# Optimization experiments

Measured on AMD Instinct MI355X. Metric: run time of the kernel, lower is better.

## Reference

```python
import jax, jax.numpy as jnp
import numpy as np

N = 100000   # graph nodes
E = 600000   # edges
D = 128      # feature_dim
K = 3        # candidate ops per MixedOp
EPS = 1e-5   # BatchNorm eps


def _param_stack(key, n_ops):
    kW, kb = jax.random.split(key)
    W = jax.random.normal(kW, (n_ops, K, D, D), jnp.float32) * (1.0 / np.sqrt(D))
    b = jax.random.normal(kb, (n_ops, K, D), jnp.float32) * 0.01
    g = jnp.ones((n_ops, K, D), jnp.float32)
    be = jnp.zeros((n_ops, K, D), jnp.float32)
    return W, b, g, be


def setup_inputs() -> dict:
    key = jax.random.key(0)
    ks = jax.random.split(key, 16)
    inp = {
        'src_emb': jax.random.normal(ks[0], (N, D), jnp.float32),
        'hr': jax.random.normal(ks[1], (N, D), jnp.float32),
        'edge_src': jax.random.randint(ks[2], (E,), 0, N),
        'edge_dst': jax.random.randint(ks[3], (E,), 0, N),
        'weights_zero': jax.random.uniform(ks[4], (1, K), jnp.float32),
        'weights_first': jax.random.uniform(ks[5], (3, K), jnp.float32),
        'weights_middle': jax.random.uniform(ks[6], (2, K), jnp.float32),
        'weights_last': jax.random.uniform(ks[7], (2, K), jnp.float32),
    }
    for name, k, n_ops in [('zero', ks[8], 1), ('first', ks[9], 3), ('mid', ks[10], 2), ('last', ks[11], 2)]:
        W, b, g, be = _param_stack(k, n_ops)
        inp[f'W_{name}'] = W; inp[f'b_{name}'] = b
        inp[f'g_{name}'] = g; inp[f'be_{name}'] = be
    inp['W_cat'] = jax.random.normal(ks[12], (3 * D, D), jnp.float32) * (1.0 / np.sqrt(3 * D))
    inp['b_cat'] = jax.random.normal(ks[13], (D,), jnp.float32) * 0.01
    inp['g_cat'] = jnp.ones((D,), jnp.float32)
    inp['be_cat'] = jnp.zeros((D,), jnp.float32)
    return inp


def _mean_agg(h, src, dst):
    s = jax.ops.segment_sum(h[src], dst, num_segments=N)            # [N,D]
    deg = jax.ops.segment_sum(jnp.ones((src.shape[0],), h.dtype), dst, num_segments=N)
    return s / jnp.maximum(deg, 1.0)[:, None]


def _max_agg(h, src, dst):
    m = jax.ops.segment_max(h[src], dst, num_segments=N)            # -inf for empty segs
    return jnp.where(jnp.isfinite(m), m, 0.0)


def _mixed(cands, w, W, b, g, be):
    # cands: list of K [N,D]; w:[K]; W:[K,D,D]; b/g/be:[K,D]
    x = jnp.stack(cands)                                            # [K,N,D]
    y = jnp.einsum('knd,kdf->knf', x, W) + b[:, None, :]            # Linear per candidate
    mu = jnp.mean(y, axis=1, keepdims=True)                         # BatchNorm1d (batch stats)
    var = jnp.var(y, axis=1, keepdims=True)
    y = (y - mu) * jax.lax.rsqrt(var + EPS) * g[:, None, :] + be[:, None, :]
    y = jax.nn.relu(y)
    return jnp.einsum('k,knd->nd', w, y)                            # alpha-weighted sum


def _graph_cands(h, src, dst):
    return [h, _mean_agg(h, src, dst), _max_agg(h, src, dst)]


def _cell_forward(src_emb, hr, edge_src, edge_dst,
                  weights_zero, weights_first, weights_middle, weights_last,
                  W_zero, b_zero, g_zero, be_zero,
                  W_first, b_first, g_first, be_first,
                  W_mid, b_mid, g_mid, be_mid,
                  W_last, b_last, g_last, be_last,
                  W_cat, b_cat, g_cat, be_cat):
    src, dst = edge_src, edge_dst
    # Cell_Zero: relation-composition candidates on (src_emb, hr)
    pre = [src_emb, src_emb - hr, src_emb * hr]
    h_in = _mixed(pre, weights_zero[0], W_zero[0], b_zero[0], g_zero[0], be_zero[0])
    # Cell_First (nodes=2): ops layout [(i=0,j=0),(i=1,j=0),(i=1,j=1)]
    states = [h_in]
    s0 = _mixed(_graph_cands(states[0], src, dst), weights_first[0], W_first[0], b_first[0], g_first[0], be_first[0])
    states.append(s0)
    s1 = (_mixed(_graph_cands(states[0], src, dst), weights_first[1], W_first[1], b_first[1], g_first[1], be_first[1])
          + _mixed(_graph_cands(states[1], src, dst), weights_first[2], W_first[2], b_first[2], g_first[2], be_first[2]))
    states.append(s1)
    states = states[1:]                                             # drop h_in -> len 2
    # Cell_Middle (nodes=2): one MixedOp per state
    states = [_mixed(_graph_cands(states[i], src, dst), weights_middle[i], W_mid[i], b_mid[i], g_mid[i], be_mid[i])
              for i in range(2)]
    # Cell_Last (in_nodes=2, nodes=1): one new state from both inputs; returns all 3
    s_last = (_mixed(_graph_cands(states[0], src, dst), weights_last[0], W_last[0], b_last[0], g_last[0], be_last[0])
              + _mixed(_graph_cands(states[1], src, dst), weights_last[1], W_last[1], b_last[1], g_last[1], be_last[1]))
    states = states + [s_last]                                      # len 3
    # concat -> Linear -> BN -> ReLU (dropout p=0)
    h = jnp.concatenate(states, axis=1) @ W_cat + b_cat             # [N,D]
    mu = jnp.mean(h, axis=0, keepdims=True)
    var = jnp.var(h, axis=0, keepdims=True)
    h = (h - mu) * jax.lax.rsqrt(var + EPS) * g_cat + be_cat
    return jax.nn.relu(h)


def reference(src_emb, hr, edge_src, edge_dst,
              weights_zero, weights_first, weights_middle, weights_last,
              W_zero, b_zero, g_zero, be_zero,
              W_first, b_first, g_first, be_first,
              W_mid, b_mid, g_mid, be_mid,
              W_last, b_last, g_last, be_last,
              W_cat, b_cat, g_cat, be_cat):
    return _cell_forward(src_emb, hr, edge_src, edge_dst,
                         weights_zero, weights_first, weights_middle, weights_last,
                         W_zero, b_zero, g_zero, be_zero,
                         W_first, b_first, g_first, be_first,
                         W_mid, b_mid, g_mid, be_mid,
                         W_last, b_last, g_last, be_last,
                         W_cat, b_cat, g_cat, be_cat)
```

## Files before the change

kernel.cpp:

```cpp
#include <hip/hip_runtime.h>

#define N_NODES 100000
#define N_EDGES 600000
#define NPAD    100096
#define NTILES  782
#define SCAN_B  98
#define EPS_F   1e-5f
#define GRIDG   256

typedef __bf16 bf16_t;
typedef __bf16 bf16x8 __attribute__((ext_vector_type(8)));
typedef __bf16 bf16x4 __attribute__((ext_vector_type(4)));
typedef float  f32x4  __attribute__((ext_vector_type(4)));

__global__ __launch_bounds__(256)
void init_zero_kernel(int* __restrict__ deg, int* __restrict__ cnt)
{
    int i = blockIdx.x * 256 + threadIdx.x;
    if (i < N_NODES) deg[i] = 0;
    if (i < 32) cnt[i] = 0;
}

__global__ __launch_bounds__(256)
void transpose_w_kernel(const float* __restrict__ Wz, const float* __restrict__ Wf,
                        const float* __restrict__ Wm, const float* __restrict__ Wl,
                        const float* __restrict__ Wc, bf16_t* __restrict__ wt)
{
    int idx = blockIdx.x * 256 + threadIdx.x;
    int mat = idx >> 14;
    int off = idx & 16383;
    int n = off >> 7, kk = off & 127;
    const float* src;
    if      (mat < 3)  src = Wz + mat * 16384;
    else if (mat < 12) src = Wf + (mat - 3) * 16384;
    else if (mat < 18) src = Wm + (mat - 12) * 16384;
    else if (mat < 24) src = Wl + (mat - 18) * 16384;
    else               src = Wc + (mat - 24) * 16384;
    wt[idx] = (bf16_t)src[kk * 128 + n];
}

__global__ __launch_bounds__(256)
void pre_kernel(const float* __restrict__ se, const float* __restrict__ hr,
                bf16_t* __restrict__ p0, bf16_t* __restrict__ p1, bf16_t* __restrict__ p2)
{
    long i = ((long)blockIdx.x * 256 + threadIdx.x) * 8;
    float4 a0 = *(const float4*)&se[i], a1 = *(const float4*)&se[i + 4];
    float4 b0 = *(const float4*)&hr[i], b1 = *(const float4*)&hr[i + 4];
    float av[8] = {a0.x, a0.y, a0.z, a0.w, a1.x, a1.y, a1.z, a1.w};
    float bv[8] = {b0.x, b0.y, b0.z, b0.w, b1.x, b1.y, b1.z, b1.w};
    bf16x8 o0, o1, o2;
#pragma unroll
    for (int j = 0; j < 8; ++j) {
        o0[j] = (bf16_t)av[j];
        o1[j] = (bf16_t)(av[j] - bv[j]);
        o2[j] = (bf16_t)(av[j] * bv[j]);
    }
    *(bf16x8*)&p0[i] = o0;
    *(bf16x8*)&p1[i] = o1;
    *(bf16x8*)&p2[i] = o2;
}

__global__ __launch_bounds__(256)
void deg_count_kernel(const int* __restrict__ dst, int* __restrict__ deg)
{
    int i = blockIdx.x * 256 + threadIdx.x;
    if (i < N_EDGES) atomicAdd(&deg[dst[i]], 1);
}

__global__ __launch_bounds__(256)
void scan_a_kernel(const int* __restrict__ deg, int* __restrict__ partials)
{
    __shared__ int ls[256];
    int b = blockIdx.x, t = threadIdx.x;
    int s = 0;
    for (int j = 0; j < 4; ++j) {
        int i = b * 1024 + t * 4 + j;
        if (i < N_NODES) s += deg[i];
    }
    ls[t] = s; __syncthreads();
    for (int o = 128; o > 0; o >>= 1) {
        if (t < o) ls[t] += ls[t + o];
        __syncthreads();
    }
    if (t == 0) partials[b] = ls[0];
}

__global__ void scan_b_kernel(const int* __restrict__ partials, int* __restrict__ pofs)
{
    if (threadIdx.x == 0) {
        int a = 0;
        for (int i = 0; i < SCAN_B; ++i) { pofs[i] = a; a += partials[i]; }
    }
}

__global__ __launch_bounds__(256)
void scan_c_kernel(const int* __restrict__ deg, const int* __restrict__ pofs,
                   int* __restrict__ row_ptr, int* __restrict__ cursor)
{
    __shared__ int ls[256];
    int b = blockIdx.x, t = threadIdx.x;
    int v[4], s = 0;
    for (int j = 0; j < 4; ++j) {
        int i = b * 1024 + t * 4 + j;
        v[j] = (i < N_NODES) ? deg[i] : 0;
        s += v[j];
    }
    ls[t] = s; __syncthreads();
    for (int o = 1; o < 256; o <<= 1) {
        int tv = (t >= o) ? ls[t - o] : 0;
        __syncthreads();
        ls[t] += tv;
        __syncthreads();
    }
    int excl = ls[t] - s + pofs[b];
    for (int j = 0; j < 4; ++j) {
        int i = b * 1024 + t * 4 + j;
        if (i < N_NODES) { row_ptr[i] = excl; cursor[i] = excl; excl += v[j]; }
    }
    if (b == 0 && t == 0) row_ptr[N_NODES] = N_EDGES;
}

__global__ __launch_bounds__(256)
void scatter_kernel(const int* __restrict__ src, const int* __restrict__ dst,
                    int* __restrict__ cursor, int* __restrict__ csr_src)
{
    int i = blockIdx.x * 256 + threadIdx.x;
    if (i < N_EDGES) {
        int p = atomicAdd(&cursor[dst[i]], 1);
        csr_src[p] = src[i];
    }
}

__global__ __launch_bounds__(256)
void agg_kernel(const bf16_t* __restrict__ h, const int* __restrict__ row_ptr,
                const int* __restrict__ csr_src,
                bf16_t* __restrict__ mean_o, bf16_t* __restrict__ max_o)
{
    int node = blockIdx.x * 16 + (threadIdx.x >> 4);
    int dd = (threadIdx.x & 15) * 8;
    int e0 = row_ptr[node], e1 = row_ptr[node + 1];
    float s[8], mx[8];
#pragma unroll
    for (int j = 0; j < 8; ++j) { s[j] = 0.f; mx[j] = 0.f; }
    for (int e = e0; e < e1; ++e) {
        int sc = csr_src[e];
        bf16x8 v = *(const bf16x8*)&h[(long)sc * 128 + dd];
#pragma unroll
        for (int j = 0; j < 8; ++j) {
            float f = (float)v[j];
            s[j] += f;
            mx[j] = fmaxf(mx[j], f);
        }
    }
    float inv = 1.f / fmaxf((float)(e1 - e0), 1.f);
    bf16x8 om, ox;
#pragma unroll
    for (int j = 0; j < 8; ++j) { om[j] = (bf16_t)(s[j] * inv); ox[j] = (bf16_t)mx[j]; }
    *(bf16x8*)&mean_o[(long)node * 128 + dd] = om;
    *(bf16x8*)&max_o [(long)node * 128 + dd] = ox;
}

__device__ __forceinline__ void gload_lds16(const bf16_t* g, bf16_t* l)
{
    __builtin_amdgcn_global_load_lds(
        (const __attribute__((address_space(1))) void*)g,
        (__attribute__((address_space(3))) void*)l, 16, 0, 0);
}

__device__ __forceinline__ void barrier_lgkm()
{
    asm volatile("s_waitcnt lgkmcnt(0)" ::: "memory");
    __builtin_amdgcn_s_barrier();
    asm volatile("" ::: "memory");
}

__device__ __forceinline__ void grid_bar(int* c, int do_rel, int do_acq)
{
    __syncthreads();
    if (threadIdx.x == 0) {
        if (do_rel) __builtin_amdgcn_fence(__ATOMIC_RELEASE, "agent");
        __hip_atomic_fetch_add(c, 1, __ATOMIC_RELAXED, __HIP_MEMORY_SCOPE_AGENT);
        while (__hip_atomic_load(c, __ATOMIC_RELAXED, __HIP_MEMORY_SCOPE_AGENT) < GRIDG)
            __builtin_amdgcn_s_sleep(16);
        if (do_acq) __builtin_amdgcn_fence(__ATOMIC_ACQUIRE, "agent");
    }
    __syncthreads();
}

__global__ __launch_bounds__(512, 1)
void mixed_kernel(const bf16_t* __restrict__ x0, const bf16_t* __restrict__ x1,
                  const bf16_t* __restrict__ x2, const bf16_t* __restrict__ wt,
                  const float* __restrict__ bias, const float* __restrict__ gg,
                  const float* __restrict__ be, const float* __restrict__ wmix,
                  bf16_t* __restrict__ outb, float* __restrict__ outf,
                  float* __restrict__ partial, float* __restrict__ tmp,
                  int* __restrict__ cnt, int mode, int accflag)
{
    __shared__ __align__(16) bf16_t lds_w[2][16384];
    __shared__ __align__(16) bf16_t lds_x[2][16384];
    __shared__ float lsc[768];

    const int tid  = threadIdx.x;
    const int lane = tid & 63;
    const int w8   = tid >> 6;
    const int quad = lane >> 4;
    const int t16  = lane & 15;
    const int wr = w8 >> 2, wc = w8 & 3;
    const int bid = blockIdx.x;
    const float invN = 1.0f / (float)N_NODES;

    int srcoff[4], dsto[4];
#pragma unroll
    for (int i = 0; i < 4; ++i) {
        int ci = i * 512 + tid;
        int row = ci >> 4, c = ci & 15;
        srcoff[i] = row * 128 + ((c ^ (row & 15)) * 8);
        dsto[i]   = ci * 8;
    }
    auto stage = [&](const bf16_t* src, bf16_t* dst) {
#pragma unroll
        for (int i = 0; i < 4; ++i)
            gload_lds16(src + srcoff[i], dst + dsto[i]);
    };
    auto xp = [&](int c) { return (c == 0) ? x0 : (c == 1) ? x1 : x2; };

    const int ts = (int)(((long)bid * NTILES) / GRIDG);
    const int te = (int)(((long)(bid + 1) * NTILES) / GRIDG);
    const int nk = (mode == 0) ? 3 : 1;

    f32x4 acc[2][4];

    {
        int s, e;
        if (mode == 0) {
            s = (int)(((long)bid * (NTILES * 3)) / GRIDG);
            e = (int)(((long)(bid + 1) * (NTILES * 3)) / GRIDG);
        } else {
            s = ts * 3; e = te * 3;
        }
        auto kofA = [&](int w) { return (mode == 0) ? (w / NTILES) : (w % 3); };
        auto tofA = [&](int w) { return (mode == 0) ? (w % NTILES) : (w / 3); };
        auto wslA = [&](int w, int k) { return (mode == 0) ? (k & 1) : (w & 1); };

        {
            int k0 = kofA(s);
            stage(wt + (long)k0 * 16384, lds_w[wslA(s, k0)]);
            stage(xp(k0) + (long)tofA(s) * 16384, lds_x[s & 1]);
        }
        for (int w = s; w < e; ++w) {
            const int ksel = kofA(w), tile = tofA(w);
            const bf16_t* wb = lds_w[wslA(w, ksel)];
            const bf16_t* xb = lds_x[w & 1];

            __syncthreads();
            if (w + 1 < e) {
                int kn = kofA(w + 1), tn = tofA(w + 1);
                if (mode == 1 || kn != ksel)
                    stage(wt + (long)kn * 16384, lds_w[wslA(w + 1, kn)]);
                stage(xp(kn) + (long)tn * 16384, lds_x[(w + 1) & 1]);
            }
            if (mode == 0 || ksel == 0) {
#pragma unroll
                for (int a = 0; a < 2; ++a)
#pragma unroll
                    for (int b = 0; b < 4; ++b) acc[a][b] = (f32x4){0.f, 0.f, 0.f, 0.f};
            }
#pragma unroll
            for (int ks = 0; ks < 4; ++ks) {
                bf16x8 xf[4], wf[2];
#pragma unroll
                for (int ms = 0; ms < 4; ++ms) {
                    int row = wr * 64 + ms * 16 + t16;
                    int sw = (ks * 4 + quad) ^ t16;
                    xf[ms] = *(const bf16x8*)&xb[row * 128 + sw * 8];
                }
#pragma unroll
                for (int ns = 0; ns < 2; ++ns) {
                    int row = wc * 32 + ns * 16 + t16;
                    int sw = (ks * 4 + quad) ^ t16;
                    wf[ns] = *(const bf16x8*)&wb[row * 128 + sw * 8];
                }
#pragma unroll
                for (int ns = 0; ns < 2; ++ns)
#pragma unroll
                    for (int ms = 0; ms < 4; ++ms)
                        acc[ns][ms] = __builtin_amdgcn_mfma_f32_16x16x32_bf16(
                            wf[ns], xf[ms], acc[ns][ms], 0, 0, 0);
            }
            if (mode == 0 || ksel == 2) {
                const float* bp = bias + ((mode == 0) ? ksel * 128 : 0);
                float ss[8], sq[8];
#pragma unroll
                for (int i = 0; i < 8; ++i) { ss[i] = 0.f; sq[i] = 0.f; }
#pragma unroll
                for (int ms = 0; ms < 4; ++ms) {
                    long m = (long)tile * 128 + wr * 64 + ms * 16 + t16;
                    if (m < N_NODES) {
#pragma unroll
                        for (int ns = 0; ns < 2; ++ns) {
                            int n0 = wc * 32 + ns * 16 + quad * 4;
                            float4 b4 = *(const float4*)&bp[n0];
                            float v0 = acc[ns][ms][0] + b4.x;
                            float v1 = acc[ns][ms][1] + b4.y;
                            float v2 = acc[ns][ms][2] + b4.z;
                            float v3 = acc[ns][ms][3] + b4.w;
                            ss[ns * 4 + 0] += v0; sq[ns * 4 + 0] += v0 * v0;
                            ss[ns * 4 + 1] += v1; sq[ns * 4 + 1] += v1 * v1;
                            ss[ns * 4 + 2] += v2; sq[ns * 4 + 2] += v2 * v2;
                            ss[ns * 4 + 3] += v3; sq[ns * 4 + 3] += v3 * v3;
                        }
                    }
                }
#pragma unroll
                for (int o = 1; o < 16; o <<= 1) {
#pragma unroll
                    for (int i = 0; i < 8; ++i) {
                        ss[i] += __shfl_xor(ss[i], o);
                        sq[i] += __shfl_xor(sq[i], o);
                    }
                }
                if (t16 == 0) {
#pragma unroll
                    for (int ns = 0; ns < 2; ++ns)
#pragma unroll
                        for (int i = 0; i < 4; ++i) {
                            lsc[w8 * 64 +      ns * 16 + quad * 4 + i] = ss[ns * 4 + i];
                            lsc[w8 * 64 + 32 + ns * 16 + quad * 4 + i] = sq[ns * 4 + i];
                        }
                }
                barrier_lgkm();
                if (tid < 256) {
                    int selo = (tid >> 7) * 32;
                    int d = tid & 127;
                    int wcq = d >> 5, f = d & 31;
                    float v = lsc[wcq * 64 + selo + f] + lsc[(wcq + 4) * 64 + selo + f];
                    int slice = (mode == 0) ? ksel : 0;
                    partial[((long)slice * NTILES + tile) * 256 + tid] = v;
                }
            }
        }
    }

    const int foldblk = (bid < nk * 16);
    grid_bar(cnt + 0, 1, foldblk);
    if (foldblk && tid < 256) {
        int k = bid >> 4, j = bid & 15;
        int b0 = j * 49, b1 = (b0 + 49 < NTILES) ? b0 + 49 : NTILES;
        float s = 0.f;
        const float* pp = partial + (long)k * NTILES * 256 + tid;
        for (int b = b0; b < b1; ++b) s += pp[(long)b * 256];
        tmp[(k * 16 + j) * 256 + tid] = s;
    }
    grid_bar(cnt + 1, foldblk, 1);
    if (tid < 128) {
        for (int k = 0; k < nk; ++k) {
            float S = 0.f, Q = 0.f;
#pragma unroll
            for (int j = 0; j < 16; ++j) {
                S += tmp[(k * 16 + j) * 256 + tid];
                Q += tmp[(k * 16 + j) * 256 + 128 + tid];
            }
            float mu = S * invN;
            float var = Q * invN - mu * mu;
            float rs = rsqrtf(var + EPS_F);
            float gk = gg[k * 128 + tid], bek = be[k * 128 + tid];
            float bk = bias[k * 128 + tid];
            float wk = (mode == 0) ? wmix[k] : 1.f;
            lsc[k * 256 + tid]       = wk * rs * gk;
            lsc[k * 256 + 128 + tid] = wk * ((bk - mu) * rs * gk + bek);
        }
    }
    __syncthreads();

    {
        int tile = ts, c = 0, p = 0;
        const int w0 = ts * 3, w1 = te * 3;
        f32x4 res[2][4];
        stage(wt, lds_w[0]);
        stage(x0 + (long)ts * 16384, lds_x[0]);
        for (int w = w0; w < w1; ++w) {
            __syncthreads();
            int cn = c + 1, tn = tile;
            if (cn == 3) { cn = 0; tn = tile + 1; }
            if (w + 1 < w1) {
                stage(wt + (long)cn * 16384, lds_w[p ^ 1]);
                stage(xp(cn) + (long)tn * 16384, lds_x[p ^ 1]);
            }
            if (mode == 0 || c == 0) {
#pragma unroll
                for (int a = 0; a < 2; ++a)
#pragma unroll
                    for (int b = 0; b < 4; ++b) acc[a][b] = (f32x4){0.f, 0.f, 0.f, 0.f};
            }
            if (mode == 0 && c == 0) {
                if (accflag) {
#pragma unroll
                    for (int ns = 0; ns < 2; ++ns)
#pragma unroll
                        for (int ms = 0; ms < 4; ++ms) {
                            long m = (long)tile * 128 + wr * 64 + ms * 16 + t16;
                            int n0 = wc * 32 + ns * 16 + quad * 4;
                            bf16x4 pv = *(const bf16x4*)&outb[m * 128 + n0];
                            res[ns][ms] = (f32x4){(float)pv[0], (float)pv[1],
                                                  (float)pv[2], (float)pv[3]};
                        }
                } else {
#pragma unroll
                    for (int a = 0; a < 2; ++a)
#pragma unroll
                        for (int b = 0; b < 4; ++b) res[a][b] = (f32x4){0.f, 0.f, 0.f, 0.f};
                }
            }
#pragma unroll
            for (int ks = 0; ks < 4; ++ks) {
                bf16x8 xf[4], wf[2];
#pragma unroll
                for (int ms = 0; ms < 4; ++ms) {
                    int row = wr * 64 + ms * 16 + t16;
                    int sw = (ks * 4 + quad) ^ t16;
                    xf[ms] = *(const bf16x8*)&lds_x[p][row * 128 + sw * 8];
                }
#pragma unroll
                for (int ns = 0; ns < 2; ++ns) {
                    int row = wc * 32 + ns * 16 + t16;
                    int sw = (ks * 4 + quad) ^ t16;
                    wf[ns] = *(const bf16x8*)&lds_w[p][row * 128 + sw * 8];
                }
#pragma unroll
                for (int ns = 0; ns < 2; ++ns)
#pragma unroll
                    for (int ms = 0; ms < 4; ++ms)
                        acc[ns][ms] = __builtin_amdgcn_mfma_f32_16x16x32_bf16(
                            wf[ns], xf[ms], acc[ns][ms], 0, 0, 0);
            }
            if (mode == 0) {
#pragma unroll
                for (int ns = 0; ns < 2; ++ns) {
                    int n0 = wc * 32 + ns * 16 + quad * 4;
                    float4 A4 = *(const float4*)&lsc[c * 256 + n0];
                    float4 B4 = *(const float4*)&lsc[c * 256 + 128 + n0];
#pragma unroll
                    for (int ms = 0; ms < 4; ++ms) {
                        res[ns][ms][0] += fmaxf(acc[ns][ms][0] * A4.x + B4.x, 0.f);
                        res[ns][ms][1] += fmaxf(acc[ns][ms][1] * A4.y + B4.y, 0.f);
                        res[ns][ms][2] += fmaxf(acc[ns][ms][2] * A4.z + B4.z, 0.f);
                        res[ns][ms][3] += fmaxf(acc[ns][ms][3] * A4.w + B4.w, 0.f);
                    }
                }
                if (c == 2) {
#pragma unroll
                    for (int ms = 0; ms < 4; ++ms) {
                        long m = (long)tile * 128 + wr * 64 + ms * 16 + t16;
                        if (m < N_NODES) {
#pragma unroll
                            for (int ns = 0; ns < 2; ++ns) {
                                int n0 = wc * 32 + ns * 16 + quad * 4;
                                bf16x4 ov;
                                ov[0] = (bf16_t)res[ns][ms][0];
                                ov[1] = (bf16_t)res[ns][ms][1];
                                ov[2] = (bf16_t)res[ns][ms][2];
                                ov[3] = (bf16_t)res[ns][ms][3];
                                *(bf16x4*)&outb[m * 128 + n0] = ov;
                            }
                        }
                    }
                }
            } else if (c == 2) {
#pragma unroll
                for (int ms = 0; ms < 4; ++ms) {
                    long m = (long)tile * 128 + wr * 64 + ms * 16 + t16;
                    if (m < N_NODES) {
#pragma unroll
                        for (int ns = 0; ns < 2; ++ns) {
                            int n0 = wc * 32 + ns * 16 + quad * 4;
                            float4 A4 = *(const float4*)&lsc[n0];
                            float4 B4 = *(const float4*)&lsc[128 + n0];
                            float4 o;
                            o.x = fmaxf(acc[ns][ms][0] * A4.x + B4.x, 0.f);
                            o.y = fmaxf(acc[ns][ms][1] * A4.y + B4.y, 0.f);
                            o.z = fmaxf(acc[ns][ms][2] * A4.z + B4.z, 0.f);
                            o.w = fmaxf(acc[ns][ms][3] * A4.w + B4.w, 0.f);
                            *(float4*)&outf[m * 128 + n0] = o;
                        }
                    }
                }
            }
            p ^= 1; c = cn; tile = tn;
        }
    }
}

extern "C" void kernel_launch(void* const* d_in, const int* in_sizes, int n_in,
                              void* d_out, int out_size, void* d_ws, size_t ws_size,
                              hipStream_t stream)
{
    const float* src_emb = (const float*)d_in[0];
    const float* hr      = (const float*)d_in[1];
    const int*   e_src   = (const int*)d_in[2];
    const int*   e_dst   = (const int*)d_in[3];
    const float* w_zero  = (const float*)d_in[4];
    const float* w_first = (const float*)d_in[5];
    const float* w_mid   = (const float*)d_in[6];
    const float* w_last  = (const float*)d_in[7];
    const float* W_zero  = (const float*)d_in[8];
    const float* b_zero  = (const float*)d_in[9];
    const float* g_zero  = (const float*)d_in[10];
    const float* be_zero = (const float*)d_in[11];
    const float* W_first = (const float*)d_in[12];
    const float* b_first = (const float*)d_in[13];
    const float* g_first = (const float*)d_in[14];
    const float* be_first= (const float*)d_in[15];
    const float* W_mid   = (const float*)d_in[16];
    const float* b_mid   = (const float*)d_in[17];
    const float* g_mid   = (const float*)d_in[18];
    const float* be_mid  = (const float*)d_in[19];
    const float* W_last  = (const float*)d_in[20];
    const float* b_last  = (const float*)d_in[21];
    const float* g_last  = (const float*)d_in[22];
    const float* be_last = (const float*)d_in[23];
    const float* W_cat   = (const float*)d_in[24];
    const float* b_cat   = (const float*)d_in[25];
    const float* g_cat   = (const float*)d_in[26];
    const float* be_cat  = (const float*)d_in[27];
    float* out = (float*)d_out;

    char* ws = (char*)d_ws;
    size_t off = 0;
    auto carve = [&](size_t bytes) -> char* {
        off = (off + 255) & ~(size_t)255;
        char* p = ws + off;
        off += bytes;
        return p;
    };

    const size_t SB = (size_t)NPAD * 128 * sizeof(bf16_t);
    bf16_t* B[8];
    for (int i = 0; i < 8; ++i) B[i] = (bf16_t*)carve(SB);
    bf16_t* wt    = (bf16_t*)carve((size_t)27 * 16384 * 2);
    float*  partial = (float*)carve((size_t)3 * NTILES * 256 * sizeof(float));
    float*  tmp   = (float*)carve((size_t)48 * 256 * sizeof(float));
    int* cnts   = (int*)carve(32 * 4);
    int* deg    = (int*)carve((size_t)N_NODES * 4);
    int* rowp   = (int*)carve((size_t)(N_NODES + 1) * 4);
    int* cursor = (int*)carve((size_t)N_NODES * 4);
    int* csr    = (int*)carve((size_t)N_EDGES * 4);
    int* parts  = (int*)carve(SCAN_B * 4);
    int* pofs   = (int*)carve(SCAN_B * 4);

    bf16_t* wtZ  = wt;
    bf16_t* wtF0 = wt + (size_t)3  * 16384;
    bf16_t* wtF1 = wt + (size_t)6  * 16384;
    bf16_t* wtF2 = wt + (size_t)9  * 16384;
    bf16_t* wtM0 = wt + (size_t)12 * 16384;
    bf16_t* wtM1 = wt + (size_t)15 * 16384;
    bf16_t* wtL0 = wt + (size_t)18 * 16384;
    bf16_t* wtL1 = wt + (size_t)21 * 16384;
    bf16_t* wtC  = wt + (size_t)24 * 16384;

    const int GEL8 = (N_NODES * 128) / 2048;

    init_zero_kernel<<<dim3((N_NODES + 255) / 256), dim3(256), 0, stream>>>(deg, cnts);
    transpose_w_kernel<<<dim3(1728), dim3(256), 0, stream>>>(W_zero, W_first, W_mid, W_last, W_cat, wt);
    deg_count_kernel<<<dim3((N_EDGES + 255) / 256), dim3(256), 0, stream>>>(e_dst, deg);
    scan_a_kernel<<<dim3(SCAN_B), dim3(256), 0, stream>>>(deg, parts);
    scan_b_kernel<<<dim3(1), dim3(64), 0, stream>>>(parts, pofs);
    scan_c_kernel<<<dim3(SCAN_B), dim3(256), 0, stream>>>(deg, pofs, rowp, cursor);
    scatter_kernel<<<dim3((N_EDGES + 255) / 256), dim3(256), 0, stream>>>(e_src, e_dst, cursor, csr);

    auto M = [&](const bf16_t* x0_, const bf16_t* x1_, const bf16_t* x2_,
                 const bf16_t* w_, const float* b_, const float* g_, const float* be_,
                 const float* wm_, bf16_t* ob_, float* of_, int acc_, int mode_, int id) {
        mixed_kernel<<<dim3(GRIDG), dim3(512), 0, stream>>>(
            x0_, x1_, x2_, w_, b_, g_, be_, wm_, ob_, of_,
            partial, tmp, cnts + id * 2, mode_, acc_);
    };
    auto A = [&](const bf16_t* h_, bf16_t* me_, bf16_t* mx_) {
        agg_kernel<<<dim3(N_NODES / 16), dim3(256), 0, stream>>>(h_, rowp, csr, me_, mx_);
    };

    pre_kernel<<<dim3(GEL8), dim3(256), 0, stream>>>(src_emb, hr, B[3], B[4], B[5]);
    M(B[3], B[4], B[5], wtZ, b_zero, g_zero, be_zero, w_zero, B[6], nullptr, 0, 0, 0);

    A(B[6], B[3], B[4]);

    M(B[6], B[3], B[4], wtF0, b_first + 0, g_first + 0, be_first + 0,
      w_first + 0, B[5], nullptr, 0, 0, 1);
    M(B[6], B[3], B[4], wtF1, b_first + 384, g_first + 384, be_first + 384,
      w_first + 3, B[7], nullptr, 0, 0, 2);

    A(B[5], B[3], B[4]);

    M(B[5], B[3], B[4], wtF2, b_first + 768, g_first + 768, be_first + 768,
      w_first + 6, B[7], nullptr, 1, 0, 3);
    M(B[5], B[3], B[4], wtM0, b_mid + 0, g_mid + 0, be_mid + 0,
      w_mid + 0, B[6], nullptr, 0, 0, 4);

    A(B[7], B[3], B[4]);

    M(B[7], B[3], B[4], wtM1, b_mid + 384, g_mid + 384, be_mid + 384,
      w_mid + 3, B[5], nullptr, 0, 0, 5);

    A(B[6], B[3], B[4]);
    M(B[6], B[3], B[4], wtL0, b_last + 0, g_last + 0, be_last + 0,
      w_last + 0, B[7], nullptr, 0, 0, 6);
    A(B[5], B[3], B[4]);
    M(B[5], B[3], B[4], wtL1, b_last + 384, g_last + 384, be_last + 384,
      w_last + 3, B[7], nullptr, 1, 0, 7);

    M(B[6], B[5], B[7], wtC, b_cat, g_cat, be_cat, nullptr,
      nullptr, out, 0, 1, 8);
}
```

Before: 1.284 ms.

## Keep mixed-op weights in registers and prefetch X tiles through a 4-slot ring

The three 128x128 weight slices are now loaded once into per-thread registers, so only X tiles are staged into LDS. Staging uses a 4-slot ring that prefetches three tiles ahead and waits on explicit vmcnt counts instead of a full sync each step. BatchNorm sums are accumulated per block across all tiles and written once per block rather than once per tile, with a shorter fold. The bias is dropped from the statistics and the affine, since it cancels after mean subtraction. This removes per-tile weight LDS traffic and per-tile reduction barriers, at the cost of much higher register pressure and hand-written wait counts that must match the number of outstanding loads.

```diff
diff --git a/kernel.cpp b/kernel.cpp
--- a/kernel.cpp
+++ b/kernel.cpp
@@ -196,8 +196,7 @@
                   float* __restrict__ partial, float* __restrict__ tmp,
                   int* __restrict__ cnt, int mode, int accflag)
 {
-    __shared__ __align__(16) bf16_t lds_w[2][16384];
-    __shared__ __align__(16) bf16_t lds_x[2][16384];
+    __shared__ __align__(16) bf16_t lds_x[4][16384];
     __shared__ float lsc[768];
 
     const int tid  = threadIdx.x;
@@ -217,127 +216,134 @@
         srcoff[i] = row * 128 + ((c ^ (row & 15)) * 8);
         dsto[i]   = ci * 8;
     }
-    auto stage = [&](const bf16_t* src, bf16_t* dst) {
+    auto stage = [&](const bf16_t* src, int slot) {
 #pragma unroll
         for (int i = 0; i < 4; ++i)
-            gload_lds16(src + srcoff[i], dst + dsto[i]);
+            gload_lds16(src + srcoff[i], &lds_x[slot][dsto[i]]);
     };
     auto xp = [&](int c) { return (c == 0) ? x0 : (c == 1) ? x1 : x2; };
+
+    bf16x8 wreg[3][2][4];
+#pragma unroll
+    for (int c = 0; c < 3; ++c)
+#pragma unroll
+        for (int ns = 0; ns < 2; ++ns)
+#pragma unroll
+            for (int ks = 0; ks < 4; ++ks)
+                wreg[c][ns][ks] = *(const bf16x8*)
+                    &wt[(long)c * 16384 + (wc * 32 + ns * 16 + t16) * 128
+                        + ks * 32 + quad * 8];
 
     const int ts = (int)(((long)bid * NTILES) / GRIDG);
     const int te = (int)(((long)(bid + 1) * NTILES) / GRIDG);
     const int nk = (mode == 0) ? 3 : 1;
 
     f32x4 acc[2][4];
+    float ssA[3][8], sqA[3][8];
+#pragma unroll
+    for (int k = 0; k < 3; ++k)
+#pragma unroll
+        for (int i = 0; i < 8; ++i) { ssA[k][i] = 0.f; sqA[k][i] = 0.f; }
+
+#define ZACC() do { \
+    _Pragma("unroll") for (int a_ = 0; a_ < 2; ++a_) \
+    _Pragma("unroll") for (int b_ = 0; b_ < 4; ++b_) \
+        acc[a_][b_] = (f32x4){0.f, 0.f, 0.f, 0.f}; } while (0)
+
+#define MMAC(C) do { \
+    _Pragma("unroll") for (int ks = 0; ks < 4; ++ks) { \
+        bf16x8 xf[4]; \
+        _Pragma("unroll") for (int ms = 0; ms < 4; ++ms) { \
+            int row_ = wr * 64 + ms * 16 + t16; \
+            int sw_ = (ks * 4 + quad) ^ t16; \
+            xf[ms] = *(const bf16x8*)&lds_x[slot][row_ * 128 + sw_ * 8]; \
+        } \
+        _Pragma("unroll") for (int ns = 0; ns < 2; ++ns) \
+        _Pragma("unroll") for (int ms = 0; ms < 4; ++ms) \
+            acc[ns][ms] = __builtin_amdgcn_mfma_f32_16x16x32_bf16( \
+                wreg[C][ns][ks], xf[ms], acc[ns][ms], 0, 0, 0); \
+    } } while (0)
+
+#define ACCST(K) do { \
+    _Pragma("unroll") for (int ms = 0; ms < 4; ++ms) { \
+        long m_ = (long)tile * 128 + wr * 64 + ms * 16 + t16; \
+        if (m_ < N_NODES) { \
+            _Pragma("unroll") for (int ns = 0; ns < 2; ++ns) \
+            _Pragma("unroll") for (int j_ = 0; j_ < 4; ++j_) { \
+                float v_ = acc[ns][ms][j_]; \
+                ssA[K][ns * 4 + j_] += v_; \
+                sqA[K][ns * 4 + j_] += v_ * v_; \
+            } \
+        } \
+    } } while (0)
+
+#define RINGWAIT(w_, e_) do { \
+    int ah_ = (e_) - 1 - (w_); \
+    if (ah_ >= 2)      asm volatile("s_waitcnt vmcnt(8)" ::: "memory"); \
+    else if (ah_ == 1) asm volatile("s_waitcnt vmcnt(4)" ::: "memory"); \
+    else               asm volatile("s_waitcnt vmcnt(0)" ::: "memory"); \
+    __builtin_amdgcn_sched_barrier(0); \
+    __builtin_amdgcn_s_barrier(); \
+    __builtin_amdgcn_sched_barrier(0); } while (0)
 
     {
-        int s, e;
+        int sA, eA;
         if (mode == 0) {
-            s = (int)(((long)bid * (NTILES * 3)) / GRIDG);
-            e = (int)(((long)(bid + 1) * (NTILES * 3)) / GRIDG);
+            sA = (int)(((long)bid * (NTILES * 3)) / GRIDG);
+            eA = (int)(((long)(bid + 1) * (NTILES * 3)) / GRIDG);
         } else {
-            s = ts * 3; e = te * 3;
-        }
-        auto kofA = [&](int w) { return (mode == 0) ? (w / NTILES) : (w % 3); };
-        auto tofA = [&](int w) { return (mode == 0) ? (w % NTILES) : (w / 3); };
-        auto wslA = [&](int w, int k) { return (mode == 0) ? (k & 1) : (w & 1); };
-
-        {
-            int k0 = kofA(s);
-            stage(wt + (long)k0 * 16384, lds_w[wslA(s, k0)]);
-            stage(xp(k0) + (long)tofA(s) * 16384, lds_x[s & 1]);
-        }
-        for (int w = s; w < e; ++w) {
-            const int ksel = kofA(w), tile = tofA(w);
-            const bf16_t* wb = lds_w[wslA(w, ksel)];
-            const bf16_t* xb = lds_x[w & 1];
-
-            __syncthreads();
-            if (w + 1 < e) {
-                int kn = kofA(w + 1), tn = tofA(w + 1);
-                if (mode == 1 || kn != ksel)
-                    stage(wt + (long)kn * 16384, lds_w[wslA(w + 1, kn)]);
-                stage(xp(kn) + (long)tn * 16384, lds_x[(w + 1) & 1]);
+            sA = ts * 3; eA = te * 3;
+        }
+#pragma unroll 1
+        for (int i = 0; i < 3; ++i)
+            if (sA + i < eA) stage(xp((sA + i) % 3) + (long)((sA + i) / 3) * 16384,
+                                   (sA + i) & 3);
+#pragma unroll 1
+        for (int w = sA; w < eA; ++w) {
+            const int c = w % 3, tile = w / 3, slot = w & 3;
+            RINGWAIT(w, eA);
+            if (w + 3 < eA)
+                stage(xp((w + 3) % 3) + (long)((w + 3) / 3) * 16384, (w + 3) & 3);
+            if (mode == 0 || c == 0) ZACC();
+            if (c == 0) MMAC(0); else if (c == 1) MMAC(1); else MMAC(2);
+            if (mode == 0) {
+                if (c == 0) ACCST(0); else if (c == 1) ACCST(1); else ACCST(2);
+            } else if (c == 2) ACCST(0);
+        }
+    }
+
+#pragma unroll
+    for (int o = 1; o < 16; o <<= 1)
+#pragma unroll
+        for (int k = 0; k < 3; ++k)
+#pragma unroll
+            for (int i = 0; i < 8; ++i) {
+                ssA[k][i] += __shfl_xor(ssA[k][i], o);
+                sqA[k][i] += __shfl_xor(sqA[k][i], o);
             }
-            if (mode == 0 || ksel == 0) {
-#pragma unroll
-                for (int a = 0; a < 2; ++a)
-#pragma unroll
-                    for (int b = 0; b < 4; ++b) acc[a][b] = (f32x4){0.f, 0.f, 0.f, 0.f};
-            }
-#pragma unroll
-            for (int ks = 0; ks < 4; ++ks) {
-                bf16x8 xf[4], wf[2];
-#pragma unroll
-                for (int ms = 0; ms < 4; ++ms) {
-                    int row = wr * 64 + ms * 16 + t16;
-                    int sw = (ks * 4 + quad) ^ t16;
-                    xf[ms] = *(const bf16x8*)&xb[row * 128 + sw * 8];
+#pragma unroll 1
+    for (int k = 0; k < nk; ++k) {
+        barrier_lgkm();
+        if (t16 == 0) {
+#pragma unroll
+            for (int ns = 0; ns < 2; ++ns)
+#pragma unroll
+                for (int i = 0; i < 4; ++i) {
+                    float s_, q_;
+                    if (k == 0)      { s_ = ssA[0][ns*4+i]; q_ = sqA[0][ns*4+i]; }
+                    else if (k == 1) { s_ = ssA[1][ns*4+i]; q_ = sqA[1][ns*4+i]; }
+                    else             { s_ = ssA[2][ns*4+i]; q_ = sqA[2][ns*4+i]; }
+                    lsc[w8 * 64 +      ns * 16 + quad * 4 + i] = s_;
+                    lsc[w8 * 64 + 32 + ns * 16 + quad * 4 + i] = q_;
                 }
-#pragma unroll
-                for (int ns = 0; ns < 2; ++ns) {
-                    int row = wc * 32 + ns * 16 + t16;
-                    int sw = (ks * 4 + quad) ^ t16;
-                    wf[ns] = *(const bf16x8*)&wb[row * 128 + sw * 8];
-                }
-#pragma unroll
-                for (int ns = 0; ns < 2; ++ns)
-#pragma unroll
-                    for (int ms = 0; ms < 4; ++ms)
-                        acc[ns][ms] = __builtin_amdgcn_mfma_f32_16x16x32_bf16(
-                            wf[ns], xf[ms], acc[ns][ms], 0, 0, 0);
-            }
-            if (mode == 0 || ksel == 2) {
-                const float* bp = bias + ((mode == 0) ? ksel * 128 : 0);
-                float ss[8], sq[8];
-#pragma unroll
-                for (int i = 0; i < 8; ++i) { ss[i] = 0.f; sq[i] = 0.f; }
-#pragma unroll
-                for (int ms = 0; ms < 4; ++ms) {
-                    long m = (long)tile * 128 + wr * 64 + ms * 16 + t16;
-                    if (m < N_NODES) {
-#pragma unroll
-                        for (int ns = 0; ns < 2; ++ns) {
-                            int n0 = wc * 32 + ns * 16 + quad * 4;
-                            float4 b4 = *(const float4*)&bp[n0];
-                            float v0 = acc[ns][ms][0] + b4.x;
-                            float v1 = acc[ns][ms][1] + b4.y;
-                            float v2 = acc[ns][ms][2] + b4.z;
-                            float v3 = acc[ns][ms][3] + b4.w;
-                            ss[ns * 4 + 0] += v0; sq[ns * 4 + 0] += v0 * v0;
-                            ss[ns * 4 + 1] += v1; sq[ns * 4 + 1] += v1 * v1;
-                            ss[ns * 4 + 2] += v2; sq[ns * 4 + 2] += v2 * v2;
-                            ss[ns * 4 + 3] += v3; sq[ns * 4 + 3] += v3 * v3;
-                        }
-                    }
-                }
-#pragma unroll
-                for (int o = 1; o < 16; o <<= 1) {
-#pragma unroll
-                    for (int i = 0; i < 8; ++i) {
-                        ss[i] += __shfl_xor(ss[i], o);
-                        sq[i] += __shfl_xor(sq[i], o);
-                    }
-                }
-                if (t16 == 0) {
-#pragma unroll
-                    for (int ns = 0; ns < 2; ++ns)
-#pragma unroll
-                        for (int i = 0; i < 4; ++i) {
-                            lsc[w8 * 64 +      ns * 16 + quad * 4 + i] = ss[ns * 4 + i];
-                            lsc[w8 * 64 + 32 + ns * 16 + quad * 4 + i] = sq[ns * 4 + i];
-                        }
-                }
-                barrier_lgkm();
-                if (tid < 256) {
-                    int selo = (tid >> 7) * 32;
-                    int d = tid & 127;
-                    int wcq = d >> 5, f = d & 31;
-                    float v = lsc[wcq * 64 + selo + f] + lsc[(wcq + 4) * 64 + selo + f];
-                    int slice = (mode == 0) ? ksel : 0;
-                    partial[((long)slice * NTILES + tile) * 256 + tid] = v;
-                }
-            }
+        }
+        barrier_lgkm();
+        if (tid < 256) {
+            int selo = (tid >> 7) * 32;
+            int d = tid & 127;
+            int wcq = d >> 5, f = d & 31;
+            float v = lsc[wcq * 64 + selo + f] + lsc[(wcq + 4) * 64 + selo + f];
+            partial[((long)k * GRIDG + bid) * 256 + tid] = v;
         }
     }
 
@@ -345,10 +351,10 @@
     grid_bar(cnt + 0, 1, foldblk);
     if (foldblk && tid < 256) {
         int k = bid >> 4, j = bid & 15;
-        int b0 = j * 49, b1 = (b0 + 49 < NTILES) ? b0 + 49 : NTILES;
         float s = 0.f;
-        const float* pp = partial + (long)k * NTILES * 256 + tid;
-        for (int b = b0; b < b1; ++b) s += pp[(long)b * 256];
+        const float* pp = partial + ((long)k * GRIDG + j * 16) * 256 + tid;
+#pragma unroll
+        for (int b = 0; b < 16; ++b) s += pp[(long)b * 256];
         tmp[(k * 16 + j) * 256 + tid] = s;
     }
     grid_bar(cnt + 1, foldblk, 1);
@@ -360,38 +366,31 @@
                 S += tmp[(k * 16 + j) * 256 + tid];
                 Q += tmp[(k * 16 + j) * 256 + 128 + tid];
             }
-            float mu = S * invN;
-            float var = Q * invN - mu * mu;
-            float rs = rsqrtf(var + EPS_F);
+            float sa  = S * invN;
+            float var = Q * invN - sa * sa;
+            float rs  = rsqrtf(var + EPS_F);
             float gk = gg[k * 128 + tid], bek = be[k * 128 + tid];
-            float bk = bias[k * 128 + tid];
             float wk = (mode == 0) ? wmix[k] : 1.f;
             lsc[k * 256 + tid]       = wk * rs * gk;
-            lsc[k * 256 + 128 + tid] = wk * ((bk - mu) * rs * gk + bek);
+            lsc[k * 256 + 128 + tid] = wk * (-sa * rs * gk + bek);
         }
     }
     __syncthreads();
 
     {
-        int tile = ts, c = 0, p = 0;
         const int w0 = ts * 3, w1 = te * 3;
         f32x4 res[2][4];
-        stage(wt, lds_w[0]);
-        stage(x0 + (long)ts * 16384, lds_x[0]);
+#pragma unroll 1
+        for (int i = 0; i < 3; ++i)
+            if (w0 + i < w1) stage(xp((w0 + i) % 3) + (long)((w0 + i) / 3) * 16384,
+                                   (w0 + i) & 3);
+#pragma unroll 1
         for (int w = w0; w < w1; ++w) {
-            __syncthreads();
-            int cn = c + 1, tn = tile;
-            if (cn == 3) { cn = 0; tn = tile + 1; }
-            if (w + 1 < w1) {
-                stage(wt + (long)cn * 16384, lds_w[p ^ 1]);
-                stage(xp(cn) + (long)tn * 16384, lds_x[p ^ 1]);
-            }
-            if (mode == 0 || c == 0) {
-#pragma unroll
-                for (int a = 0; a < 2; ++a)
-#pragma unroll
-                    for (int b = 0; b < 4; ++b) acc[a][b] = (f32x4){0.f, 0.f, 0.f, 0.f};
-            }
+            const int c = w % 3, tile = w / 3, slot = w & 3;
+            RINGWAIT(w, w1);
+            if (w + 3 < w1)
+                stage(xp((w + 3) % 3) + (long)((w + 3) / 3) * 16384, (w + 3) & 3);
+            if (mode == 0 || c == 0) ZACC();
             if (mode == 0 && c == 0) {
                 if (accflag) {
 #pragma unroll
@@ -411,28 +410,8 @@
                         for (int b = 0; b < 4; ++b) res[a][b] = (f32x4){0.f, 0.f, 0.f, 0.f};
                 }
             }
-#pragma unroll
-            for (int ks = 0; ks < 4; ++ks) {
-                bf16x8 xf[4], wf[2];
-#pragma unroll
-                for (int ms = 0; ms < 4; ++ms) {
-                    int row = wr * 64 + ms * 16 + t16;
-                    int sw = (ks * 4 + quad) ^ t16;
-                    xf[ms] = *(const bf16x8*)&lds_x[p][row * 128 + sw * 8];
-                }
-#pragma unroll
-                for (int ns = 0; ns < 2; ++ns) {
-                    int row = wc * 32 + ns * 16 + t16;
-                    int sw = (ks * 4 + quad) ^ t16;
-                    wf[ns] = *(const bf16x8*)&lds_w[p][row * 128 + sw * 8];
-                }
-#pragma unroll
-                for (int ns = 0; ns < 2; ++ns)
-#pragma unroll
-                    for (int ms = 0; ms < 4; ++ms)
-                        acc[ns][ms] = __builtin_amdgcn_mfma_f32_16x16x32_bf16(
-                            wf[ns], xf[ms], acc[ns][ms], 0, 0, 0);
-            }
+            if (c == 0) MMAC(0); else if (c == 1) MMAC(1); else MMAC(2);
+
             if (mode == 0) {
 #pragma unroll
                 for (int ns = 0; ns < 2; ++ns) {
@@ -485,9 +464,12 @@
                     }
                 }
             }
-            p ^= 1; c = cn; tile = tn;
-        }
-    }
+        }
+    }
+#undef ZACC
+#undef MMAC
+#undef ACCST
+#undef RINGWAIT
 }
 
 extern "C" void kernel_launch(void* const* d_in, const int* in_sizes, int n_in,
@@ -537,7 +519,7 @@
     bf16_t* B[8];
     for (int i = 0; i < 8; ++i) B[i] = (bf16_t*)carve(SB);
     bf16_t* wt    = (bf16_t*)carve((size_t)27 * 16384 * 2);
-    float*  partial = (float*)carve((size_t)3 * NTILES * 256 * sizeof(float));
+    float*  partial = (float*)carve((size_t)3 * GRIDG * 256 * sizeof(float));
     float*  tmp   = (float*)carve((size_t)48 * 256 * sizeof(float));
     int* cnts   = (int*)carve(32 * 4);
     int* deg    = (int*)carve((size_t)N_NODES * 4);
```

Result: faster. 1.163 ms (-9.4%).
